# Kernel optimization log

Hardware: AMD Instinct MI355X
Metric: run time of the kernel (lower is better)

## Reference

```python
import jax, jax.numpy as jnp
import numpy as np

BATCH, INPUT_SIZE, HIDDEN = 128, 32, 1024


def setup_inputs() -> dict:
    key = jax.random.key(0)
    k1, k2, k3, k4 = jax.random.split(key, 4)
    idx = jax.random.randint(k1, (BATCH,), 0, INPUT_SIZE)
    inp = jax.nn.one_hot(idx, INPUT_SIZE, dtype=jnp.float32)  # one-hot per assert
    state = jax.random.normal(k2, (1, BATCH, HIDDEN), dtype=jnp.float32)
    weight = jax.random.normal(k3, (HIDDEN, HIDDEN, INPUT_SIZE), dtype=jnp.float32) * 0.02
    bias = jax.random.normal(k4, (HIDDEN, INPUT_SIZE), dtype=jnp.float32) * 0.02
    return {"input": inp, "state": state, "weight": weight, "bias": bias}


def reference(input, state, weight, bias):
    # Faithful to SRUCell.forward: one-hot selection of per-input weight/bias,
    # expressed as contractions (same math, no [B,H,H,I] materialization).
    hx = state[0]                                             # [B, H]
    # rec_temp = sum_j sum_i weight[h,j,i] * input[b,i] * hx[b,j]
    rec_temp = jnp.einsum('hji,bi,bj->bh', weight, input, hx)  # [B, H]
    trial_bias = jnp.einsum('hi,bi->bh', bias, input)          # [B, H]
    hy = hx + rec_temp + trial_bias
    return hy[None, ...]                                       # [1, B, H]
```

## Files before the change

kernel.cpp:

```cpp
#include <hip/hip_runtime.h>


constexpr int B  = 128;
constexpr int I  = 32;
constexpr int H  = 1024;
constexpr int K  = H * I;
constexpr int BM = 64;
constexpr int BK = 64;
constexpr int SPLIT = 32;
constexpr int KC = K / SPLIT;
constexpr int NT = KC / BK;

typedef short  short8 __attribute__((ext_vector_type(8)));
typedef unsigned int uint4v __attribute__((ext_vector_type(4)));
typedef float  f32x4  __attribute__((ext_vector_type(4)));

__device__ __forceinline__ unsigned short f2bf(float f) {
    unsigned u = __builtin_bit_cast(unsigned, f);
    return (unsigned short)((u + 0x7FFFu + ((u >> 16) & 1u)) >> 16);
}

__device__ __forceinline__ void argmax32(const float* __restrict__ inp, int b,
                                         int& ib, float& vb) {
    float best = inp[b * I];
    int bi = 0;
#pragma unroll
    for (int i = 1; i < I; ++i) {
        float v = inp[b * I + i];
        if (v > best) { best = v; bi = i; }
    }
    ib = bi; vb = best;
}

__global__ __launch_bounds__(256) void sru_init_kernel(
    const float* __restrict__ inp, const float* __restrict__ hx,
    const float* __restrict__ bias, float* __restrict__ out) {
    int e = blockIdx.x * 256 + threadIdx.x;
    int b = e >> 10, h = e & (H - 1);
    int ib; float v; argmax32(inp, b, ib, v);
    out[e] = hx[e] + v * bias[h * I + ib];
}

__global__ __launch_bounds__(256) void sru_reduce_kernel(
    const float* __restrict__ inp, const float* __restrict__ hx,
    const float* __restrict__ bias, const float* __restrict__ partial,
    float* __restrict__ out) {
    const int b  = blockIdx.x;
    const int h4 = threadIdx.x * 4;
    int ib; float v; argmax32(inp, b, ib, v);
    float4 s = *reinterpret_cast<const float4*>(&hx[b * H + h4]);
    s.x += v * bias[(h4 + 0) * I + ib];
    s.y += v * bias[(h4 + 1) * I + ib];
    s.z += v * bias[(h4 + 2) * I + ib];
    s.w += v * bias[(h4 + 3) * I + ib];
#pragma unroll
    for (int sp = 0; sp < SPLIT; ++sp) {
        float4 p = *reinterpret_cast<const float4*>(
            &partial[((size_t)sp * B + b) * H + h4]);
        s.x += p.x; s.y += p.y; s.z += p.z; s.w += p.w;
    }
    *reinterpret_cast<float4*>(&out[b * H + h4]) = s;
}

template <bool USE_WS>
__global__ __launch_bounds__(512, 4) void sru_gemm_kernel(
    const float* __restrict__ inp, const float* __restrict__ hx,
    const float* __restrict__ w, float* __restrict__ out) {
    __shared__ __align__(16) unsigned short As[2][BM * BK];
    __shared__ __align__(16) unsigned short hxs[B * 32];
    __shared__ int   idxs[B];
    __shared__ float vals[B];

    const int tid = threadIdx.x;
    const int h0  = blockIdx.x * BM;
    const int by  = blockIdx.y;
    const int kc0 = by * KC;

    if (tid < B) {
        int ib; float vb; argmax32(inp, tid, ib, vb);
        idxs[tid] = ib; vals[tid] = vb;
    }
    __syncthreads();

    {
        int b  = tid >> 2;
        int c0 = (tid & 3) * 8;
        const float* p = hx + b * H + by * 32 + c0;
        float4 v0 = *reinterpret_cast<const float4*>(p);
        float4 v1 = *reinterpret_cast<const float4*>(p + 4);
        float vb = vals[b];
        short8 s;
        s[0] = (short)f2bf(v0.x * vb); s[1] = (short)f2bf(v0.y * vb);
        s[2] = (short)f2bf(v0.z * vb); s[3] = (short)f2bf(v0.w * vb);
        s[4] = (short)f2bf(v1.x * vb); s[5] = (short)f2bf(v1.y * vb);
        s[6] = (short)f2bf(v1.z * vb); s[7] = (short)f2bf(v1.w * vb);
        *reinterpret_cast<short8*>(&hxs[b * 32 + c0]) = s;
    }

    const int arow = tid >> 3;
    const int ag   = tid & 7;
    const float* ap = w + (size_t)(h0 + arow) * K + kc0 + ag * 8;
    const int awoff = arow * 64 + (ag ^ (arow & 7)) * 8;

    float4 r0, r1;
    auto loadA = [&](int t) {
        const float* p = ap + t * BK;
        r0 = *reinterpret_cast<const float4*>(p);
        r1 = *reinterpret_cast<const float4*>(p + 4);
    };
    auto writeA = [&](int buf) {
        short8 s;
        s[0] = (short)f2bf(r0.x); s[1] = (short)f2bf(r0.y);
        s[2] = (short)f2bf(r0.z); s[3] = (short)f2bf(r0.w);
        s[4] = (short)f2bf(r1.x); s[5] = (short)f2bf(r1.y);
        s[6] = (short)f2bf(r1.z); s[7] = (short)f2bf(r1.w);
        *reinterpret_cast<short8*>(&As[buf][awoff]) = s;
    };

    const int lane = tid & 63;
    const int wid  = tid >> 6;
    const int wm = wid & 1;
    const int wn = wid >> 1;
    const int kg = lane >> 4;

    int aoff[2][2];
#pragma unroll
    for (int fm = 0; fm < 2; ++fm) {
        int r = wm * 32 + fm * 16 + (lane & 15);
#pragma unroll
        for (int ks = 0; ks < 2; ++ks)
            aoff[fm][ks] = r * 64 + (((ks * 4 + kg) ^ (r & 7))) * 8;
    }

    int bcol[2];
    uint4v msk[2];
#pragma unroll
    for (int fn = 0; fn < 2; ++fn) {
        bcol[fn] = wn * 32 + fn * 16 + (lane & 15);
        int rel = idxs[bcol[fn]] - kg * 8;
        uint4v m;
#pragma unroll
        for (int q = 0; q < 4; ++q) {
            unsigned lo = (rel == 2 * q)     ? 0xFFFFu : 0u;
            unsigned hi = (rel == 2 * q + 1) ? 0xFFFFu : 0u;
            m[q] = lo | (hi << 16);
        }
        msk[fn] = m;
    }

    f32x4 acc[2][2];
#pragma unroll
    for (int fm = 0; fm < 2; ++fm)
#pragma unroll
        for (int fn = 0; fn < 2; ++fn)
            acc[fm][fn] = f32x4{0.f, 0.f, 0.f, 0.f};

    auto compute = [&](int buf, int t) {
#pragma unroll
        for (int ks = 0; ks < 2; ++ks) {
            short8 af[2], xf[2];
#pragma unroll
            for (int fm = 0; fm < 2; ++fm)
                af[fm] = *reinterpret_cast<const short8*>(&As[buf][aoff[fm][ks]]);
#pragma unroll
            for (int fn = 0; fn < 2; ++fn) {
                unsigned hv = hxs[bcol[fn] * 32 + t * 2 + ks];
                unsigned hv32 = hv | (hv << 16);
                uint4v xd;
#pragma unroll
                for (int q = 0; q < 4; ++q) xd[q] = msk[fn][q] & hv32;
                xf[fn] = __builtin_bit_cast(short8, xd);
            }
#pragma unroll
            for (int fm = 0; fm < 2; ++fm)
#pragma unroll
                for (int fn = 0; fn < 2; ++fn)
                    acc[fm][fn] = __builtin_amdgcn_mfma_f32_16x16x32_bf16(
                        af[fm], xf[fn], acc[fm][fn], 0, 0, 0);
        }
    };

    loadA(0);
    __syncthreads();
    writeA(0);
    loadA(1);
    __syncthreads();
    int cur = 0;
    for (int t = 0; t < NT; ++t) {
        if (t + 1 < NT) {
            writeA(cur ^ 1);
            if (t + 2 < NT) loadA(t + 2);
        }
        compute(cur, t);
        __syncthreads();
        cur ^= 1;
    }

    if constexpr (USE_WS) {
        float* pp = out + (size_t)by * (B * H);
#pragma unroll
        for (int fm = 0; fm < 2; ++fm) {
#pragma unroll
            for (int fn = 0; fn < 2; ++fn) {
                int n  = bcol[fn];
                int m0 = wm * 32 + fm * 16 + (lane >> 4) * 4;
                float4 vv = {acc[fm][fn][0], acc[fm][fn][1],
                             acc[fm][fn][2], acc[fm][fn][3]};
                *reinterpret_cast<float4*>(&pp[(size_t)n * H + h0 + m0]) = vv;
            }
        }
    } else {
#pragma unroll
        for (int fm = 0; fm < 2; ++fm) {
#pragma unroll
            for (int fn = 0; fn < 2; ++fn) {
                int n  = bcol[fn];
                int m0 = wm * 32 + fm * 16 + (lane >> 4) * 4;
#pragma unroll
                for (int rr = 0; rr < 4; ++rr)
                    atomicAdd(&out[(size_t)n * H + h0 + m0 + rr], acc[fm][fn][rr]);
            }
        }
    }
}

extern "C" void kernel_launch(void* const* d_in, const int* in_sizes, int n_in,
                              void* d_out, int out_size, void* d_ws, size_t ws_size,
                              hipStream_t stream) {
    const float* inp    = (const float*)d_in[0];
    const float* state  = (const float*)d_in[1];
    const float* weight = (const float*)d_in[2];
    const float* bias   = (const float*)d_in[3];
    float* out = (float*)d_out;

    float* partial = (float*)d_ws;
    const size_t need = (size_t)SPLIT * B * H * sizeof(float);

    if (ws_size >= need) {
        sru_gemm_kernel<true><<<dim3(H / BM, SPLIT), 512, 0, stream>>>(
            inp, state, weight, partial);
        sru_reduce_kernel<<<B, 256, 0, stream>>>(
            inp, state, bias, partial, out);
    } else {
        sru_init_kernel<<<(B * H) / 256, 256, 0, stream>>>(inp, state, bias, out);
        sru_gemm_kernel<false><<<dim3(H / BM, SPLIT), 512, 0, stream>>>(
            inp, state, weight, out);
    }
}
```

Baseline: 35.28 us.

## Stream weight fragments directly to registers per wave, drop LDS weight staging

The GEMM kernel no longer stages converted weight tiles in shared memory with block-wide barriers. Each wave owns 16 hidden rows and loads its weight fragments straight from global memory into registers, two steps ahead, converting to bf16 in registers. It covers all 128 batch columns with 8 accumulators. The hx tile is transposed in LDS to suit the new access pattern, and the reduce kernel is split across twice as many smaller blocks. This removes LDS traffic and per-iteration syncs, at the cost of more registers per thread, lower occupancy bounds, and weight loads that are less coalesced.

```diff
diff --git a/kernel.cpp b/kernel.cpp
--- a/kernel.cpp
+++ b/kernel.cpp
@@ -5,11 +5,9 @@
 constexpr int I  = 32;
 constexpr int H  = 1024;
 constexpr int K  = H * I;
-constexpr int BM = 64;
-constexpr int BK = 64;
 constexpr int SPLIT = 32;
-constexpr int KC = K / SPLIT;
-constexpr int NT = KC / BK;
+constexpr int JC = H / SPLIT;
+constexpr int WPB = 4;
 
 typedef short  short8 __attribute__((ext_vector_type(8)));
 typedef unsigned int uint4v __attribute__((ext_vector_type(4)));
@@ -41,12 +39,12 @@
     out[e] = hx[e] + v * bias[h * I + ib];
 }
 
-__global__ __launch_bounds__(256) void sru_reduce_kernel(
+__global__ __launch_bounds__(128) void sru_reduce_kernel(
     const float* __restrict__ inp, const float* __restrict__ hx,
     const float* __restrict__ bias, const float* __restrict__ partial,
     float* __restrict__ out) {
-    const int b  = blockIdx.x;
-    const int h4 = threadIdx.x * 4;
+    const int b  = blockIdx.x >> 1;
+    const int h4 = (blockIdx.x & 1) * 512 + threadIdx.x * 4;
     int ib; float v; argmax32(inp, b, ib, v);
     float4 s = *reinterpret_cast<const float4*>(&hx[b * H + h4]);
     s.x += v * bias[(h4 + 0) * I + ib];
@@ -63,18 +61,21 @@
 }
 
 template <bool USE_WS>
-__global__ __launch_bounds__(512, 4) void sru_gemm_kernel(
+__global__ __launch_bounds__(256, 2) void sru_gemm_kernel(
     const float* __restrict__ inp, const float* __restrict__ hx,
     const float* __restrict__ w, float* __restrict__ out) {
-    __shared__ __align__(16) unsigned short As[2][BM * BK];
-    __shared__ __align__(16) unsigned short hxs[B * 32];
+    __shared__ unsigned short hxs[JC * B];
     __shared__ int   idxs[B];
     __shared__ float vals[B];
 
-    const int tid = threadIdx.x;
-    const int h0  = blockIdx.x * BM;
-    const int by  = blockIdx.y;
-    const int kc0 = by * KC;
+    const int tid  = threadIdx.x;
+    const int lane = tid & 63;
+    const int wid  = tid >> 6;
+    const int by   = blockIdx.y;
+    const int j0   = by * JC;
+    const int h0   = blockIdx.x * (16 * WPB) + wid * 16;
+    const int r16  = lane & 15;
+    const int kg   = lane >> 4;
 
     if (tid < B) {
         int ib; float vb; argmax32(inp, tid, ib, vb);
@@ -83,61 +84,25 @@
     __syncthreads();
 
     {
-        int b  = tid >> 2;
-        int c0 = (tid & 3) * 8;
-        const float* p = hx + b * H + by * 32 + c0;
-        float4 v0 = *reinterpret_cast<const float4*>(p);
-        float4 v1 = *reinterpret_cast<const float4*>(p + 4);
+        int b  = tid >> 1;
+        int jh = (tid & 1) * 16;
+        const float* p = hx + b * H + j0 + jh;
         float vb = vals[b];
-        short8 s;
-        s[0] = (short)f2bf(v0.x * vb); s[1] = (short)f2bf(v0.y * vb);
-        s[2] = (short)f2bf(v0.z * vb); s[3] = (short)f2bf(v0.w * vb);
-        s[4] = (short)f2bf(v1.x * vb); s[5] = (short)f2bf(v1.y * vb);
-        s[6] = (short)f2bf(v1.z * vb); s[7] = (short)f2bf(v1.w * vb);
-        *reinterpret_cast<short8*>(&hxs[b * 32 + c0]) = s;
+#pragma unroll
+        for (int q = 0; q < 4; ++q) {
+            float4 v = *reinterpret_cast<const float4*>(p + q * 4);
+            hxs[(jh + q * 4 + 0) * B + b] = f2bf(v.x * vb);
+            hxs[(jh + q * 4 + 1) * B + b] = f2bf(v.y * vb);
+            hxs[(jh + q * 4 + 2) * B + b] = f2bf(v.z * vb);
+            hxs[(jh + q * 4 + 3) * B + b] = f2bf(v.w * vb);
+        }
     }
+    __syncthreads();
 
-    const int arow = tid >> 3;
-    const int ag   = tid & 7;
-    const float* ap = w + (size_t)(h0 + arow) * K + kc0 + ag * 8;
-    const int awoff = arow * 64 + (ag ^ (arow & 7)) * 8;
-
-    float4 r0, r1;
-    auto loadA = [&](int t) {
-        const float* p = ap + t * BK;
-        r0 = *reinterpret_cast<const float4*>(p);
-        r1 = *reinterpret_cast<const float4*>(p + 4);
-    };
-    auto writeA = [&](int buf) {
-        short8 s;
-        s[0] = (short)f2bf(r0.x); s[1] = (short)f2bf(r0.y);
-        s[2] = (short)f2bf(r0.z); s[3] = (short)f2bf(r0.w);
-        s[4] = (short)f2bf(r1.x); s[5] = (short)f2bf(r1.y);
-        s[6] = (short)f2bf(r1.z); s[7] = (short)f2bf(r1.w);
-        *reinterpret_cast<short8*>(&As[buf][awoff]) = s;
-    };
-
-    const int lane = tid & 63;
-    const int wid  = tid >> 6;
-    const int wm = wid & 1;
-    const int wn = wid >> 1;
-    const int kg = lane >> 4;
-
-    int aoff[2][2];
+    uint4v msk[8];
 #pragma unroll
-    for (int fm = 0; fm < 2; ++fm) {
-        int r = wm * 32 + fm * 16 + (lane & 15);
-#pragma unroll
-        for (int ks = 0; ks < 2; ++ks)
-            aoff[fm][ks] = r * 64 + (((ks * 4 + kg) ^ (r & 7))) * 8;
-    }
-
-    int bcol[2];
-    uint4v msk[2];
-#pragma unroll
-    for (int fn = 0; fn < 2; ++fn) {
-        bcol[fn] = wn * 32 + fn * 16 + (lane & 15);
-        int rel = idxs[bcol[fn]] - kg * 8;
+    for (int g = 0; g < 8; ++g) {
+        int rel = idxs[g * 16 + r16] - kg * 8;
         uint4v m;
 #pragma unroll
         for (int q = 0; q < 4; ++q) {
@@ -145,81 +110,60 @@
             unsigned hi = (rel == 2 * q + 1) ? 0xFFFFu : 0u;
             m[q] = lo | (hi << 16);
         }
-        msk[fn] = m;
+        msk[g] = m;
     }
 
-    f32x4 acc[2][2];
+    const float* ap = w + (size_t)(h0 + r16) * K + (size_t)j0 * I + kg * 8;
+
+    f32x4 acc[8];
 #pragma unroll
-    for (int fm = 0; fm < 2; ++fm)
+    for (int g = 0; g < 8; ++g) acc[g] = f32x4{0.f, 0.f, 0.f, 0.f};
+
+    float4 c0 = *reinterpret_cast<const float4*>(ap);
+    float4 c1 = *reinterpret_cast<const float4*>(ap + 4);
+    float4 n0 = *reinterpret_cast<const float4*>(ap + 32);
+    float4 n1 = *reinterpret_cast<const float4*>(ap + 36);
+    float4 t0 = c0, t1 = c1;
+
+    for (int s = 0; s < JC; ++s) {
+        if (s + 2 < JC) {
+            const float* p = ap + (size_t)(s + 2) * 32;
+            t0 = *reinterpret_cast<const float4*>(p);
+            t1 = *reinterpret_cast<const float4*>(p + 4);
+        }
+        short8 af;
+        af[0] = (short)f2bf(c0.x); af[1] = (short)f2bf(c0.y);
+        af[2] = (short)f2bf(c0.z); af[3] = (short)f2bf(c0.w);
+        af[4] = (short)f2bf(c1.x); af[5] = (short)f2bf(c1.y);
+        af[6] = (short)f2bf(c1.z); af[7] = (short)f2bf(c1.w);
 #pragma unroll
-        for (int fn = 0; fn < 2; ++fn)
-            acc[fm][fn] = f32x4{0.f, 0.f, 0.f, 0.f};
-
-    auto compute = [&](int buf, int t) {
+        for (int g = 0; g < 8; ++g) {
+            unsigned hv = hxs[s * B + g * 16 + r16];
+            unsigned hv32 = hv | (hv << 16);
+            uint4v xd;
 #pragma unroll
-        for (int ks = 0; ks < 2; ++ks) {
-            short8 af[2], xf[2];
-#pragma unroll
-            for (int fm = 0; fm < 2; ++fm)
-                af[fm] = *reinterpret_cast<const short8*>(&As[buf][aoff[fm][ks]]);
-#pragma unroll
-            for (int fn = 0; fn < 2; ++fn) {
-                unsigned hv = hxs[bcol[fn] * 32 + t * 2 + ks];
-                unsigned hv32 = hv | (hv << 16);
-                uint4v xd;
-#pragma unroll
-                for (int q = 0; q < 4; ++q) xd[q] = msk[fn][q] & hv32;
-                xf[fn] = __builtin_bit_cast(short8, xd);
-            }
-#pragma unroll
-            for (int fm = 0; fm < 2; ++fm)
-#pragma unroll
-                for (int fn = 0; fn < 2; ++fn)
-                    acc[fm][fn] = __builtin_amdgcn_mfma_f32_16x16x32_bf16(
-                        af[fm], xf[fn], acc[fm][fn], 0, 0, 0);
+            for (int q = 0; q < 4; ++q) xd[q] = msk[g][q] & hv32;
+            acc[g] = __builtin_amdgcn_mfma_f32_16x16x32_bf16(
+                af, __builtin_bit_cast(short8, xd), acc[g], 0, 0, 0);
         }
-    };
-
-    loadA(0);
-    __syncthreads();
-    writeA(0);
-    loadA(1);
-    __syncthreads();
-    int cur = 0;
-    for (int t = 0; t < NT; ++t) {
-        if (t + 1 < NT) {
-            writeA(cur ^ 1);
-            if (t + 2 < NT) loadA(t + 2);
-        }
-        compute(cur, t);
-        __syncthreads();
-        cur ^= 1;
+        c0 = n0; c1 = n1; n0 = t0; n1 = t1;
     }
 
     if constexpr (USE_WS) {
         float* pp = out + (size_t)by * (B * H);
 #pragma unroll
-        for (int fm = 0; fm < 2; ++fm) {
-#pragma unroll
-            for (int fn = 0; fn < 2; ++fn) {
-                int n  = bcol[fn];
-                int m0 = wm * 32 + fm * 16 + (lane >> 4) * 4;
-                float4 vv = {acc[fm][fn][0], acc[fm][fn][1],
-                             acc[fm][fn][2], acc[fm][fn][3]};
-                *reinterpret_cast<float4*>(&pp[(size_t)n * H + h0 + m0]) = vv;
-            }
+        for (int g = 0; g < 8; ++g) {
+            int b = g * 16 + r16;
+            float4 vv = {acc[g][0], acc[g][1], acc[g][2], acc[g][3]};
+            *reinterpret_cast<float4*>(&pp[(size_t)b * H + h0 + kg * 4]) = vv;
         }
     } else {
 #pragma unroll
-        for (int fm = 0; fm < 2; ++fm) {
+        for (int g = 0; g < 8; ++g) {
+            int b = g * 16 + r16;
 #pragma unroll
-            for (int fn = 0; fn < 2; ++fn) {
-                int n  = bcol[fn];
-                int m0 = wm * 32 + fm * 16 + (lane >> 4) * 4;
-#pragma unroll
-                for (int rr = 0; rr < 4; ++rr)
-                    atomicAdd(&out[(size_t)n * H + h0 + m0 + rr], acc[fm][fn][rr]);
-            }
+            for (int rr = 0; rr < 4; ++rr)
+                atomicAdd(&out[(size_t)b * H + h0 + kg * 4 + rr], acc[g][rr]);
         }
     }
 }
@@ -237,13 +181,13 @@
     const size_t need = (size_t)SPLIT * B * H * sizeof(float);
 
     if (ws_size >= need) {
-        sru_gemm_kernel<true><<<dim3(H / BM, SPLIT), 512, 0, stream>>>(
+        sru_gemm_kernel<true><<<dim3(H / (16 * WPB), SPLIT), 256, 0, stream>>>(
             inp, state, weight, partial);
-        sru_reduce_kernel<<<B, 256, 0, stream>>>(
+        sru_reduce_kernel<<<2 * B, 128, 0, stream>>>(
             inp, state, bias, partial, out);
     } else {
         sru_init_kernel<<<(B * H) / 256, 256, 0, stream>>>(inp, state, bias, out);
-        sru_gemm_kernel<false><<<dim3(H / BM, SPLIT), 512, 0, stream>>>(
+        sru_gemm_kernel<false><<<dim3(H / (16 * WPB), SPLIT), 256, 0, stream>>>(
             inp, state, weight, out);
     }
 }
```

New measurement: 34.58 us. 1.02x faster.
